# Kernel tuning notes

Hardware: AMD Instinct MI355X
Metric: run time of the kernel (lower is better)

## Reference

```python
import jax, jax.numpy as jnp
import numpy as np

N, M = 4096, 256

def setup_inputs() -> dict:
    key = jax.random.key(0)
    k1, k2 = jax.random.split(key)
    y_pred = jax.random.normal(k1, (N, M), dtype=jnp.float32)
    y = jax.random.normal(k2, (N, 1), dtype=jnp.float32)
    return {"y_pred": y_pred, "y": y}

def reference(y_pred, y):
    n, m = y_pred.shape
    # MAE term: mean(|y_pred - y|), y broadcast over ensemble dim
    mae_loss = jnp.mean(jnp.abs(y_pred - y))
    # Ensemble spread term: sum_{i,k,l} |x[i,k] - x[i,l]| / (n * 2 * m^2)
    # pairwise diffs: [n, m, m]
    pair = jnp.abs(y_pred[:, None, :] - y_pred[:, :, None])
    mix_loss = jnp.sum(pair) / (n * 2 * m ** 2)
    return mae_loss - mix_loss
```

## Files before the change

kernel.cpp:

```cpp
#include <hip/hip_runtime.h>


constexpr int N_ROWS = 4096;
constexpr int M_COLS = 256;
constexpr int ROWS_PER_BLOCK = 4;

__global__ __launch_bounds__(256)
void crps_kernel(const float* __restrict__ y_pred,
                 const float* __restrict__ y,
                 float* __restrict__ out) {
    __shared__ __align__(16) float4 rows[ROWS_PER_BLOCK][M_COLS / 4];
    __shared__ float wsum[ROWS_PER_BLOCK];

    const int wave = threadIdx.x >> 6;
    const int lane = threadIdx.x & 63;
    const int row  = blockIdx.x * ROWS_PER_BLOCK + wave;

    const float4* gp = reinterpret_cast<const float4*>(y_pred + row * M_COLS);
    const float4 xk = gp[lane];
    rows[wave][lane] = xk;
    const float yi = y[row];
    __syncthreads();

    float m0 = 0.0f, m1 = 0.0f, m2 = 0.0f, m3 = 0.0f;
    const float4* r4 = rows[wave];
    #pragma unroll 8
    for (int l = 0; l < M_COLS / 4; ++l) {
        const float4 v = r4[l];
        m0 += fabsf(xk.x - v.x) + fabsf(xk.x - v.y) + fabsf(xk.x - v.z) + fabsf(xk.x - v.w);
        m1 += fabsf(xk.y - v.x) + fabsf(xk.y - v.y) + fabsf(xk.y - v.z) + fabsf(xk.y - v.w);
        m2 += fabsf(xk.z - v.x) + fabsf(xk.z - v.y) + fabsf(xk.z - v.z) + fabsf(xk.z - v.w);
        m3 += fabsf(xk.w - v.x) + fabsf(xk.w - v.y) + fabsf(xk.w - v.z) + fabsf(xk.w - v.w);
    }
    const float mix = (m0 + m1) + (m2 + m3);

    const float mae = fabsf(xk.x - yi) + fabsf(xk.y - yi)
                    + fabsf(xk.z - yi) + fabsf(xk.w - yi);

    constexpr float mae_scale = 1.0f / ((float)N_ROWS * (float)M_COLS);
    constexpr float mix_scale = 1.0f / (2.0f * (float)N_ROWS * (float)M_COLS * (float)M_COLS);
    float part = mae * mae_scale - mix * mix_scale;

    #pragma unroll
    for (int off = 32; off > 0; off >>= 1)
        part += __shfl_down(part, off, 64);

    if (lane == 0) wsum[wave] = part;
    __syncthreads();
    if (threadIdx.x == 0) {
        atomicAdd(out, (wsum[0] + wsum[1]) + (wsum[2] + wsum[3]));
    }
}

extern "C" void kernel_launch(void* const* d_in, const int* in_sizes, int n_in,
                              void* d_out, int out_size, void* d_ws, size_t ws_size,
                              hipStream_t stream) {
    const float* y_pred = (const float*)d_in[0];
    const float* y      = (const float*)d_in[1];
    float* out          = (float*)d_out;

    hipMemsetAsync(out, 0, sizeof(float), stream);

    crps_kernel<<<N_ROWS / ROWS_PER_BLOCK, 256, 0, stream>>>(y_pred, y, out);
}
```

Baseline: 76.33 us.

## Exploit pairwise symmetry, fuse abs-add via inline asm, and use last-block reduction

```diff
diff --git a/kernel.cpp b/kernel.cpp
--- a/kernel.cpp
+++ b/kernel.cpp
@@ -4,42 +4,64 @@
 constexpr int N_ROWS = 4096;
 constexpr int M_COLS = 256;
 constexpr int ROWS_PER_BLOCK = 4;
+constexpr int NUM_BLOCKS = N_ROWS / ROWS_PER_BLOCK;
+
+__device__ __forceinline__ void abs_acc(float& m, float a, float b) {
+    float t = a - b;
+    asm("v_add_f32 %0, %0, |%1|" : "+v"(m) : "v"(t));
+}
 
 __global__ __launch_bounds__(256)
 void crps_kernel(const float* __restrict__ y_pred,
                  const float* __restrict__ y,
+                 float* __restrict__ ws_partial,
+                 unsigned int* __restrict__ ws_count,
                  float* __restrict__ out) {
-    __shared__ __align__(16) float4 rows[ROWS_PER_BLOCK][M_COLS / 4];
+    __shared__ __align__(16) float4 rows[ROWS_PER_BLOCK][2 * M_COLS / 4];
     __shared__ float wsum[ROWS_PER_BLOCK];
+    __shared__ bool is_last;
 
     const int wave = threadIdx.x >> 6;
     const int lane = threadIdx.x & 63;
     const int row  = blockIdx.x * ROWS_PER_BLOCK + wave;
 
-    const float4* gp = reinterpret_cast<const float4*>(y_pred + row * M_COLS);
-    const float4 xk = gp[lane];
-    rows[wave][lane] = xk;
+    const float4 xk = reinterpret_cast<const float4*>(y_pred + row * M_COLS)[lane];
+    rows[wave][lane]      = xk;
+    rows[wave][lane + 64] = xk;
     const float yi = y[row];
-    __syncthreads();
 
-    float m0 = 0.0f, m1 = 0.0f, m2 = 0.0f, m3 = 0.0f;
-    const float4* r4 = rows[wave];
-    #pragma unroll 8
-    for (int l = 0; l < M_COLS / 4; ++l) {
-        const float4 v = r4[l];
-        m0 += fabsf(xk.x - v.x) + fabsf(xk.x - v.y) + fabsf(xk.x - v.z) + fabsf(xk.x - v.w);
-        m1 += fabsf(xk.y - v.x) + fabsf(xk.y - v.y) + fabsf(xk.y - v.z) + fabsf(xk.y - v.w);
-        m2 += fabsf(xk.z - v.x) + fabsf(xk.z - v.y) + fabsf(xk.z - v.z) + fabsf(xk.z - v.w);
-        m3 += fabsf(xk.w - v.x) + fabsf(xk.w - v.y) + fabsf(xk.w - v.z) + fabsf(xk.w - v.w);
+    const float xo[4] = {xk.x, xk.y, xk.z, xk.w};
+
+    float mae = 0.0f;
+    #pragma unroll
+    for (int j = 0; j < 4; ++j) abs_acc(mae, xo[j], yi);
+
+    float m = 0.0f, m32 = 0.0f;
+    abs_acc(m, xo[0], xo[1]); abs_acc(m, xo[0], xo[2]); abs_acc(m, xo[0], xo[3]);
+    abs_acc(m, xo[1], xo[2]); abs_acc(m, xo[1], xo[3]); abs_acc(m, xo[2], xo[3]);
+
+    const float4* r4 = &rows[wave][lane];
+    #pragma unroll
+    for (int s = 1; s <= 31; ++s) {
+        const float4 v = r4[s];
+        #pragma unroll
+        for (int j = 0; j < 4; ++j) {
+            abs_acc(m, xo[j], v.x); abs_acc(m, xo[j], v.y);
+            abs_acc(m, xo[j], v.z); abs_acc(m, xo[j], v.w);
+        }
     }
-    const float mix = (m0 + m1) + (m2 + m3);
-
-    const float mae = fabsf(xk.x - yi) + fabsf(xk.y - yi)
-                    + fabsf(xk.z - yi) + fabsf(xk.w - yi);
+    {
+        const float4 v = r4[32];
+        #pragma unroll
+        for (int j = 0; j < 4; ++j) {
+            abs_acc(m32, xo[j], v.x); abs_acc(m32, xo[j], v.y);
+            abs_acc(m32, xo[j], v.z); abs_acc(m32, xo[j], v.w);
+        }
+    }
 
     constexpr float mae_scale = 1.0f / ((float)N_ROWS * (float)M_COLS);
-    constexpr float mix_scale = 1.0f / (2.0f * (float)N_ROWS * (float)M_COLS * (float)M_COLS);
-    float part = mae * mae_scale - mix * mix_scale;
+    constexpr float inv_NM2   = 1.0f / ((float)N_ROWS * (float)M_COLS * (float)M_COLS);
+    float part = mae * mae_scale - (m + 0.5f * m32) * inv_NM2;
 
     #pragma unroll
     for (int off = 32; off > 0; off >>= 1)
@@ -48,7 +70,24 @@
     if (lane == 0) wsum[wave] = part;
     __syncthreads();
     if (threadIdx.x == 0) {
-        atomicAdd(out, (wsum[0] + wsum[1]) + (wsum[2] + wsum[3]));
+        ws_partial[blockIdx.x] = (wsum[0] + wsum[1]) + (wsum[2] + wsum[3]);
+        __threadfence();
+        const unsigned int prev = atomicAdd(ws_count, 1u);
+        is_last = (prev == NUM_BLOCKS - 1);
+    }
+    __syncthreads();
+
+    if (is_last) {
+        __threadfence();
+        const float4 p4 = reinterpret_cast<const float4*>(ws_partial)[threadIdx.x];
+        float v = (p4.x + p4.y) + (p4.z + p4.w);
+        #pragma unroll
+        for (int off = 32; off > 0; off >>= 1)
+            v += __shfl_down(v, off, 64);
+        if (lane == 0) wsum[wave] = v;
+        __syncthreads();
+        if (threadIdx.x == 0)
+            *out = (wsum[0] + wsum[1]) + (wsum[2] + wsum[3]);
     }
 }
 
@@ -58,8 +97,10 @@
     const float* y_pred = (const float*)d_in[0];
     const float* y      = (const float*)d_in[1];
     float* out          = (float*)d_out;
+    float* ws_partial   = (float*)d_ws;
+    unsigned int* ws_count = (unsigned int*)((char*)d_ws + NUM_BLOCKS * sizeof(float));
 
-    hipMemsetAsync(out, 0, sizeof(float), stream);
+    hipMemsetAsync(ws_count, 0, sizeof(unsigned int), stream);
 
-    crps_kernel<<<N_ROWS / ROWS_PER_BLOCK, 256, 0, stream>>>(y_pred, y, out);
+    crps_kernel<<<NUM_BLOCKS, 256, 0, stream>>>(y_pred, y, ws_partial, ws_count, out);
 }
```

Result: slower. 81.71 us (+7.0%).
